# Kernel tuning notes

Hardware: AMD Instinct MI355X
Metric: run time of the kernel (lower is better)

Reference implementation:

```python
import jax, jax.numpy as jnp
import numpy as np

THETA = 10000.0
N_HEADS = 16


def setup_inputs() -> dict:
    key = jax.random.key(0)
    kx, kq, kk, kv, ko = jax.random.split(key, 5)
    B, S, D = 2, 2048, 1024
    std = np.sqrt(2.0 / (D + D))
    def mk_w(k):
        # trunc_normal in [-3*std, 3*std], stored as [in_features, out_features]
        return jax.random.truncated_normal(k, -3.0, 3.0, (D, D), jnp.float32) * std
    return {
        "x": jax.random.normal(kx, (B, S, D), dtype=jnp.float32),
        "token_positions": jnp.arange(S, dtype=jnp.int64) if jax.config.jax_enable_x64 else jnp.arange(S, dtype=jnp.int32),
        "WQ": mk_w(kq),
        "WK": mk_w(kk),
        "WV": mk_w(kv),
        "WO": mk_w(ko),
    }


def _rope(x, pos, theta):
    # x: [B, H, S, d_k]; pos: [S]
    d_k = x.shape[-1]
    freq = 1.0 / theta ** (jnp.arange(0, d_k, 2, dtype=jnp.float32) / d_k)  # [d_k//2]
    ang = pos.astype(jnp.float32)[:, None] * freq                            # [S, d_k//2]
    cos, sin = jnp.cos(ang), jnp.sin(ang)
    xp = x.reshape(x.shape[:-1] + (d_k // 2, 2))
    x0, x1 = xp[..., 0], xp[..., 1]
    r0 = cos * x0 - sin * x1
    r1 = sin * x0 + cos * x1
    return jnp.stack([r0, r1], axis=-1).reshape(x.shape)


def reference(x, token_positions, WQ, WK, WV, WO):
    B, S, D = x.shape
    H = N_HEADS
    dk = D // H
    # Linear in source computes y = x @ W.T (W stored [in, out], used transposed)
    def proj(W):
        return jnp.einsum('oi,bsi->bso', W, x).reshape(B, S, H, dk).transpose(0, 2, 1, 3)
    Q = proj(WQ)  # [B, H, S, dk]
    K = proj(WK)
    V = proj(WV)
    Q = _rope(Q, token_positions, THETA)
    K = _rope(K, token_positions, THETA)
    scores = jnp.einsum('bhqd,bhkd->bhqk', Q, K) / np.sqrt(dk).astype(np.float32)
    causal = jnp.tril(jnp.ones((S, S), dtype=bool))
    scores = jnp.where(causal, scores, jnp.float32(-1e9))
    w = jax.nn.softmax(scores, axis=-1)
    out = jnp.einsum('bhqk,bhkd->bhqd', w, V)
    out = out.transpose(0, 2, 1, 3).reshape(B, S, D)
    return jnp.einsum('oi,bsi->bso', WO, out)
```

## Files before the change

kernel.cpp:

```cpp
#include <hip/hip_runtime.h>
#include <hip/hip_bf16.h>

#define S_LEN   2048
#define D_MODEL 1024
#define NH      16
#define DKH     64
#define BATCH   2
#define BS_ROWS 4096

typedef unsigned short u16;
typedef __attribute__((ext_vector_type(4))) float f32x4;
typedef __attribute__((ext_vector_type(8))) short bf16x8;

__device__ __forceinline__ float bf2f(u16 u) {
  union { unsigned int i; float f; } v; v.i = ((unsigned int)u) << 16; return v.f;
}
__device__ __forceinline__ u16 f2bf(float f) {
  union { __hip_bfloat16 h; u16 u; } cv; cv.h = __float2bfloat16(f); return cv.u;
}
__device__ __forceinline__ f32x4 mfma16(bf16x8 a, bf16x8 b, f32x4 c) {
  return __builtin_amdgcn_mfma_f32_16x16x32_bf16(a, b, c, 0, 0, 0);
}
__device__ __forceinline__ void gl_lds16(const u16* g, u16* l) {
  __builtin_amdgcn_global_load_lds(
      (const __attribute__((address_space(1))) void*)g,
      (__attribute__((address_space(3))) void*)l, 16, 0, 0);
}

__global__ void cvt_all(const float* __restrict__ x,
                        const float* __restrict__ wq, const float* __restrict__ wk,
                        const float* __restrict__ wv, const float* __restrict__ wo,
                        u16* __restrict__ xb, u16* __restrict__ wqb, u16* __restrict__ wkb,
                        u16* __restrict__ wvb, u16* __restrict__ wob) {
  int seg = blockIdx.y;
  const float* src; u16* dst;
  if (seg < 4)      { src = x + (size_t)seg * (1u << 20); dst = xb + (size_t)seg * (1u << 20); }
  else if (seg == 4){ src = wq; dst = wqb; }
  else if (seg == 5){ src = wk; dst = wkb; }
  else if (seg == 6){ src = wv; dst = wvb; }
  else              { src = wo; dst = wob; }
  int i = blockIdx.x * 256 + threadIdx.x;
  float4 v = reinterpret_cast<const float4*>(src)[i];
  ushort4 o;
  o.x = f2bf(v.x); o.y = f2bf(v.y); o.z = f2bf(v.z); o.w = f2bf(v.w);
  reinterpret_cast<ushort4*>(dst)[i] = o;
}

#define BM 128
#define BN 128
#define BKK 64

__global__ __launch_bounds__(256) void gemm_bt(
    const u16* __restrict__ A,
    const u16* __restrict__ B0, const u16* __restrict__ B1, const u16* __restrict__ B2,
    u16* __restrict__ C0, u16* __restrict__ C1, u16* __restrict__ C2,
    float* __restrict__ Cf,
    int M, int N, int K, int out_f32)
{
  __shared__ __align__(16) u16 As[BM * BKK];
  __shared__ __align__(16) u16 Bs[BN * BKK];

  const int z = blockIdx.z;
  const u16* Bm = (z == 0) ? B0 : ((z == 1) ? B1 : B2);
  u16* Cb = (z == 0) ? C0 : ((z == 1) ? C1 : C2);

  const int tid = threadIdx.x;
  const int l = tid & 63, w = tid >> 6;
  const int lr = l & 15, lg = l >> 4;
  const int m0 = blockIdx.y * BM, n0 = blockIdx.x * BN;
  const int wr = w >> 1, wc = w & 1;

  f32x4 acc[4][4];
#pragma unroll
  for (int mi = 0; mi < 4; ++mi)
#pragma unroll
    for (int nj = 0; nj < 4; ++nj)
      acc[mi][nj] = (f32x4){0.f, 0.f, 0.f, 0.f};

  for (int k0 = 0; k0 < K; k0 += BKK) {
    __syncthreads();
#pragma unroll
    for (int i = 0; i < 4; ++i) {
      int Dc = w * 256 + i * 64 + l;
      int row = Dc >> 3;
      int c = (Dc & 7) ^ (row & 7);
      gl_lds16(A  + (size_t)(m0 + row) * K + k0 + c * 8, As + (w * 256 + i * 64) * 8);
      gl_lds16(Bm + (size_t)(n0 + row) * K + k0 + c * 8, Bs + (w * 256 + i * 64) * 8);
    }
    __syncthreads();

    bf16x8 af[2][4], bfr[2][4];
#pragma unroll
    for (int kk = 0; kk < 2; ++kk)
#pragma unroll
      for (int mi = 0; mi < 4; ++mi) {
        int rowa = wr * 64 + mi * 16 + lr;
        int ck = kk * 4 + lg;
        af[kk][mi] = *(const bf16x8*)&As[rowa * BKK + (((ck) ^ (rowa & 7)) << 3)];
        int rowb = wc * 64 + mi * 16 + lr;
        bfr[kk][mi] = *(const bf16x8*)&Bs[rowb * BKK + (((ck) ^ (rowb & 7)) << 3)];
      }
#pragma unroll
    for (int kk = 0; kk < 2; ++kk)
#pragma unroll
      for (int mi = 0; mi < 4; ++mi)
#pragma unroll
        for (int nj = 0; nj < 4; ++nj)
          acc[mi][nj] = mfma16(af[kk][mi], bfr[kk][nj], acc[mi][nj]);
  }

#pragma unroll
  for (int mi = 0; mi < 4; ++mi)
#pragma unroll
    for (int nj = 0; nj < 4; ++nj)
#pragma unroll
      for (int r = 0; r < 4; ++r) {
        int row = m0 + wr * 64 + mi * 16 + lg * 4 + r;
        int col = n0 + wc * 64 + nj * 16 + lr;
        float v = acc[mi][nj][r];
        if (out_f32) Cf[(size_t)row * N + col] = v;
        else         Cb[(size_t)row * N + col] = f2bf(v);
      }
}

__global__ void rope_pack(const u16* __restrict__ Yq, const u16* __restrict__ Yk,
                          const u16* __restrict__ Yv, const int* __restrict__ pos,
                          u16* __restrict__ Qb, u16* __restrict__ Kb, u16* __restrict__ Vt)
{
  int t = blockIdx.x * blockDim.x + threadIdx.x;
  if (t >= BS_ROWS * (D_MODEL / 2)) return;
  int pi = t & 511;
  int r  = t >> 9;
  int h = pi >> 5, j = pi & 31;
  int b = r >> 11, s = r & (S_LEN - 1);
  int p = pos[s];

  float freq = exp2f(-(float)j * 0.41524101186092028f);
  float ang = (float)p * freq;
  float sn, cs;
  sincosf(ang, &sn, &cs);

  int base = r * D_MODEL + pi * 2;
  float q0 = bf2f(Yq[base]), q1 = bf2f(Yq[base + 1]);
  float k0 = bf2f(Yk[base]), k1 = bf2f(Yk[base + 1]);
  float v0 = bf2f(Yv[base]), v1 = bf2f(Yv[base + 1]);

  const float QS = 0.18033688011112042f;
  float qr0 = (cs * q0 - sn * q1) * QS;
  float qr1 = (sn * q0 + cs * q1) * QS;
  float kr0 = cs * k0 - sn * k1;
  float kr1 = sn * k0 + cs * k1;

  int bh = b * NH + h;
  size_t qidx = ((size_t)bh * S_LEN + s) * DKH + 2 * j;
  ushort2 qo; qo.x = f2bf(qr0); qo.y = f2bf(qr1);
  ushort2 ko; ko.x = f2bf(kr0); ko.y = f2bf(kr1);
  *reinterpret_cast<ushort2*>(Qb + qidx) = qo;
  *reinterpret_cast<ushort2*>(Kb + qidx) = ko;
  Vt[((size_t)bh * DKH + 2 * j)     * S_LEN + s] = f2bf(v0);
  Vt[((size_t)bh * DKH + 2 * j + 1) * S_LEN + s] = f2bf(v1);
}

__global__ __launch_bounds__(256) void attn_fwd(
    const u16* __restrict__ Qb, const u16* __restrict__ Kb,
    const u16* __restrict__ Vt, u16* __restrict__ Ob)
{
  const int f = blockIdx.x;
  const int xcd = f & 7, slot = f >> 3;
  const int bh = xcd * 4 + (slot >> 4);
  const int p  = slot & 15;
  const int qbh = 31 - p, qbl = p;
  const int b = bh >> 4, h = bh & 15;
  const int tid = threadIdx.x, l = tid & 63, w = tid >> 6;
  const int lr = l & 15, lg = l >> 4;

  __shared__ __align__(16) u16 Ks[2][64 * 64];
  __shared__ __align__(16) u16 Vs[2][64 * 64];
  __shared__ __align__(16) u16 Ps[4][16 * 64];

  const u16* Qh = Qb + (size_t)bh * S_LEN * DKH;
  const u16* Kh = Kb + (size_t)bh * S_LEN * DKH;
  const u16* Vh = Vt + (size_t)bh * DKH * S_LEN;

  const int q0h = qbh * 64 + w * 16;
  const int q0l = qbl * 64 + w * 16;

  bf16x8 qfh[2], qfl[2];
#pragma unroll
  for (int kk = 0; kk < 2; ++kk) {
    qfh[kk] = *(const bf16x8*)(Qh + (size_t)(q0h + lr) * DKH + kk * 32 + lg * 8);
    qfl[kk] = *(const bf16x8*)(Qh + (size_t)(q0l + lr) * DKH + kk * 32 + lg * 8);
  }

  f32x4 oh[4], ol[4];
  float mh[4], ml[4], lh[4], ll[4];
#pragma unroll
  for (int r = 0; r < 4; ++r) {
    mh[r] = -INFINITY; ml[r] = -INFINITY; lh[r] = 0.f; ll[r] = 0.f;
  }
#pragma unroll
  for (int nb = 0; nb < 4; ++nb) {
    oh[nb] = (f32x4){0.f, 0.f, 0.f, 0.f};
    ol[nb] = (f32x4){0.f, 0.f, 0.f, 0.f};
  }

#define STAGE(buf, tt) do {                                                        \
    int kv0s = (tt) * 64;                                                          \
    _Pragma("unroll")                                                              \
    for (int i = 0; i < 2; ++i) {                                                  \
      int Dc = w * 128 + i * 64 + l;                                               \
      int row = Dc >> 3;                                                           \
      int c = (Dc & 7) ^ (row & 7);                                                \
      gl_lds16(Kh + (size_t)(kv0s + row) * DKH + c * 8, &Ks[buf][(w * 128 + i * 64) * 8]); \
      gl_lds16(Vh + (size_t)row * S_LEN + kv0s + c * 8, &Vs[buf][(w * 128 + i * 64) * 8]); \
    }                                                                              \
  } while (0)

  auto compute = [&](int cur, int kv0, const bf16x8 (&qf)[2], f32x4 (&oacc)[4],
                     float (&m)[4], float (&lsum)[4], int q0, bool diag) {
    f32x4 sf[4];
#pragma unroll
    for (int nj = 0; nj < 4; ++nj) {
      f32x4 a = (f32x4){0.f, 0.f, 0.f, 0.f};
#pragma unroll
      for (int kk = 0; kk < 2; ++kk) {
        int brow = nj * 16 + lr;
        bf16x8 kf = *(const bf16x8*)&Ks[cur][brow * 64 + (((kk * 4 + lg) ^ (brow & 7)) << 3)];
        a = mfma16(qf[kk], kf, a);
      }
      sf[nj] = a;
    }
    if (diag) {
#pragma unroll
      for (int nj = 0; nj < 4; ++nj)
#pragma unroll
        for (int r = 0; r < 4; ++r) {
          int colg = kv0 + nj * 16 + lr;
          int rowg = q0 + lg * 4 + r;
          if (colg > rowg) sf[nj][r] = -1e30f;
        }
    }
    float pm[4];
#pragma unroll
    for (int r = 0; r < 4; ++r) {
      float v = fmaxf(fmaxf(sf[0][r], sf[1][r]), fmaxf(sf[2][r], sf[3][r]));
      v = fmaxf(v, __shfl_xor(v, 1));
      v = fmaxf(v, __shfl_xor(v, 2));
      v = fmaxf(v, __shfl_xor(v, 4));
      v = fmaxf(v, __shfl_xor(v, 8));
      pm[r] = v;
    }
    bool need = false;
#pragma unroll
    for (int r = 0; r < 4; ++r) need = need || (pm[r] > m[r] + 8.f);
    if (__any(need)) {
#pragma unroll
      for (int r = 0; r < 4; ++r) {
        float mn = fmaxf(m[r], pm[r]);
        float sc = exp2f(m[r] - mn);
        m[r] = mn;
        lsum[r] *= sc;
#pragma unroll
        for (int nb = 0; nb < 4; ++nb) oacc[nb][r] *= sc;
      }
    }
    float ps[4] = {0.f, 0.f, 0.f, 0.f};
#pragma unroll
    for (int nj = 0; nj < 4; ++nj)
#pragma unroll
      for (int r = 0; r < 4; ++r) {
        float pv = exp2f(sf[nj][r] - m[r]);
        sf[nj][r] = pv;
        ps[r] += pv;
      }
#pragma unroll
    for (int r = 0; r < 4; ++r) lsum[r] += ps[r];

#pragma unroll
    for (int nj = 0; nj < 4; ++nj)
#pragma unroll
      for (int r = 0; r < 4; ++r) {
        int row = lg * 4 + r, col = nj * 16 + lr;
        int ck = col >> 3;
        Ps[w][row * 64 + ((ck ^ (row & 7)) << 3) + (col & 7)] = f2bf(sf[nj][r]);
      }
#pragma unroll
    for (int kk = 0; kk < 2; ++kk) {
      bf16x8 pa = *(const bf16x8*)&Ps[w][lr * 64 + (((kk * 4 + lg) ^ (lr & 7)) << 3)];
#pragma unroll
      for (int nb = 0; nb < 4; ++nb) {
        int vrow = nb * 16 + lr;
        bf16x8 vf = *(const bf16x8*)&Vs[cur][vrow * 64 + (((kk * 4 + lg) ^ (vrow & 7)) << 3)];
        oacc[nb] = mfma16(pa, vf, oacc[nb]);
      }
    }
  };

  const int nt = 32 - p;
  STAGE(0, 0);
  __syncthreads();
  int cur = 0;
  for (int t = 0; t < nt; ++t) {
    if (t + 1 < nt) STAGE(cur ^ 1, t + 1);
    const int kv0 = t * 64;
    compute(cur, kv0, qfh, oh, mh, lh, q0h, t == qbh);
    if (t <= p) compute(cur, kv0, qfl, ol, ml, ll, q0l, t == qbl);
    __syncthreads();
    cur ^= 1;
  }
#undef STAGE

  auto finish = [&](f32x4 (&oacc)[4], float (&lsum)[4], int q0) {
    float inv[4];
#pragma unroll
    for (int r = 0; r < 4; ++r) {
      float v = lsum[r];
      v += __shfl_xor(v, 1); v += __shfl_xor(v, 2);
      v += __shfl_xor(v, 4); v += __shfl_xor(v, 8);
      inv[r] = 1.0f / v;
    }
#pragma unroll
    for (int nb = 0; nb < 4; ++nb)
#pragma unroll
      for (int r = 0; r < 4; ++r) {
        int sg = q0 + lg * 4 + r;
        int dg = nb * 16 + lr;
        Ob[(size_t)b * S_LEN * D_MODEL + (size_t)sg * D_MODEL + h * DKH + dg] =
            f2bf(oacc[nb][r] * inv[r]);
      }
  };
  finish(oh, lh, q0h);
  finish(ol, ll, q0l);
}

extern "C" void kernel_launch(void* const* d_in, const int* in_sizes, int n_in,
                              void* d_out, int out_size, void* d_ws, size_t ws_size,
                              hipStream_t stream) {
  const float* x   = (const float*)d_in[0];
  const int*   pos = (const int*)d_in[1];
  const float* WQ  = (const float*)d_in[2];
  const float* WK  = (const float*)d_in[3];
  const float* WV  = (const float*)d_in[4];
  const float* WO  = (const float*)d_in[5];

  char* ws = (char*)d_ws;
  u16* xb  = (u16*)(ws);
  u16* wqb = (u16*)(ws + (size_t)(8)  * 1048576);
  u16* wkb = (u16*)(ws + (size_t)(10) * 1048576);
  u16* wvb = (u16*)(ws + (size_t)(12) * 1048576);
  u16* wob = (u16*)(ws + (size_t)(14) * 1048576);
  u16* Yq  = (u16*)(ws + (size_t)(16) * 1048576);
  u16* Yk  = (u16*)(ws + (size_t)(24) * 1048576);
  u16* Yv  = (u16*)(ws + (size_t)(32) * 1048576);
  u16* Qb  = (u16*)(ws + (size_t)(40) * 1048576);
  u16* Kb  = (u16*)(ws + (size_t)(48) * 1048576);
  u16* Vt  = (u16*)(ws + (size_t)(56) * 1048576);
  u16* Ob  = (u16*)(ws + (size_t)(64) * 1048576);

  cvt_all<<<dim3(1024, 8), 256, 0, stream>>>(x, WQ, WK, WV, WO, xb, wqb, wkb, wvb, wob);

  gemm_bt<<<dim3(D_MODEL / BN, BS_ROWS / BM, 3), 256, 0, stream>>>(
      xb, wqb, wkb, wvb, Yq, Yk, Yv, nullptr, BS_ROWS, D_MODEL, D_MODEL, 0);

  rope_pack<<<(BS_ROWS * (D_MODEL / 2)) / 256, 256, 0, stream>>>(
      Yq, Yk, Yv, pos, Qb, Kb, Vt);

  attn_fwd<<<dim3(512), 256, 0, stream>>>(Qb, Kb, Vt, Ob);

  gemm_bt<<<dim3(D_MODEL / BN, BS_ROWS / BM, 1), 256, 0, stream>>>(
      Ob, wob, wob, wob, nullptr, nullptr, nullptr, (float*)d_out,
      BS_ROWS, D_MODEL, D_MODEL, 1);
}
```

Before: 249.1 us.

## Split V transpose into tiled LDS kernel and use one query block per attention workgroup

The strided scatter of V into the transposed layout moves out of rope_pack into a dedicated LDS-tiled transpose kernel, so both its reads and its writes are coalesced. The attention kernel drops the paired high/low query-block scheme and instead launches 1024 workgroups, one 64-row query block each, ordered longest-first with a launch-bounds occupancy hint. This cuts per-block register pressure and raises parallelism, but each block loads its own K/V tiles, so pairs no longer share them. It also gives up the explicit XCD-aware head placement and adds one extra kernel launch.

After: 238.2 us. -4.4%, faster.

```diff
diff --git a/kernel.cpp b/kernel.cpp
--- a/kernel.cpp
+++ b/kernel.cpp
@@ -9,6 +9,7 @@
 #define BS_ROWS 4096
 
 typedef unsigned short u16;
+typedef unsigned int   u32;
 typedef __attribute__((ext_vector_type(4))) float f32x4;
 typedef __attribute__((ext_vector_type(8))) short bf16x8;
 
@@ -124,8 +125,8 @@
 }
 
 __global__ void rope_pack(const u16* __restrict__ Yq, const u16* __restrict__ Yk,
-                          const u16* __restrict__ Yv, const int* __restrict__ pos,
-                          u16* __restrict__ Qb, u16* __restrict__ Kb, u16* __restrict__ Vt)
+                          const int* __restrict__ pos,
+                          u16* __restrict__ Qb, u16* __restrict__ Kb)
 {
   int t = blockIdx.x * blockDim.x + threadIdx.x;
   if (t >= BS_ROWS * (D_MODEL / 2)) return;
@@ -143,7 +144,6 @@
   int base = r * D_MODEL + pi * 2;
   float q0 = bf2f(Yq[base]), q1 = bf2f(Yq[base + 1]);
   float k0 = bf2f(Yk[base]), k1 = bf2f(Yk[base + 1]);
-  float v0 = bf2f(Yv[base]), v1 = bf2f(Yv[base + 1]);
 
   const float QS = 0.18033688011112042f;
   float qr0 = (cs * q0 - sn * q1) * QS;
@@ -157,19 +157,46 @@
   ushort2 ko; ko.x = f2bf(kr0); ko.y = f2bf(kr1);
   *reinterpret_cast<ushort2*>(Qb + qidx) = qo;
   *reinterpret_cast<ushort2*>(Kb + qidx) = ko;
-  Vt[((size_t)bh * DKH + 2 * j)     * S_LEN + s] = f2bf(v0);
-  Vt[((size_t)bh * DKH + 2 * j + 1) * S_LEN + s] = f2bf(v1);
-}
-
-__global__ __launch_bounds__(256) void attn_fwd(
+}
+
+__global__ __launch_bounds__(256) void transpose_v(const u16* __restrict__ Yv,
+                                                   u16* __restrict__ Vt)
+{
+  __shared__ u32 T[64][65];
+  const int sb = blockIdx.x;
+  const int bh = blockIdx.y;
+  const int b = bh >> 4, h = bh & 15;
+  const int t = threadIdx.x;
+  const int s0 = sb * 64;
+
+#pragma unroll
+  for (int pass = 0; pass < 2; ++pass) {
+    int row = pass * 32 + (t >> 3);
+    int c0 = (t & 7) * 8;
+    bf16x8 v = *(const bf16x8*)(Yv + (size_t)(b * S_LEN + s0 + row) * D_MODEL + h * DKH + c0);
+#pragma unroll
+    for (int i = 0; i < 8; ++i) T[row][c0 + i] = (u32)(u16)v[i];
+  }
+  __syncthreads();
+
+  const int d = t >> 2, ch = t & 3;
+  bf16x8 o0, o1;
+#pragma unroll
+  for (int i = 0; i < 8; ++i) o0[i] = (short)(u16)T[ch * 16 + i][d];
+#pragma unroll
+  for (int i = 0; i < 8; ++i) o1[i] = (short)(u16)T[ch * 16 + 8 + i][d];
+  u16* dst = Vt + ((size_t)bh * DKH + d) * S_LEN + s0 + ch * 16;
+  *(bf16x8*)dst = o0;
+  *(bf16x8*)(dst + 8) = o1;
+}
+
+__global__ __launch_bounds__(256, 4) void attn_fwd(
     const u16* __restrict__ Qb, const u16* __restrict__ Kb,
     const u16* __restrict__ Vt, u16* __restrict__ Ob)
 {
   const int f = blockIdx.x;
-  const int xcd = f & 7, slot = f >> 3;
-  const int bh = xcd * 4 + (slot >> 4);
-  const int p  = slot & 15;
-  const int qbh = 31 - p, qbl = p;
+  const int qb = 31 - (f >> 5);
+  const int bh = f & 31;
   const int b = bh >> 4, h = bh & 15;
   const int tid = threadIdx.x, l = tid & 63, w = tid >> 6;
   const int lr = l & 15, lg = l >> 4;
@@ -182,27 +209,19 @@
   const u16* Kh = Kb + (size_t)bh * S_LEN * DKH;
   const u16* Vh = Vt + (size_t)bh * DKH * S_LEN;
 
-  const int q0h = qbh * 64 + w * 16;
-  const int q0l = qbl * 64 + w * 16;
-
-  bf16x8 qfh[2], qfl[2];
-#pragma unroll
-  for (int kk = 0; kk < 2; ++kk) {
-    qfh[kk] = *(const bf16x8*)(Qh + (size_t)(q0h + lr) * DKH + kk * 32 + lg * 8);
-    qfl[kk] = *(const bf16x8*)(Qh + (size_t)(q0l + lr) * DKH + kk * 32 + lg * 8);
-  }
-
-  f32x4 oh[4], ol[4];
-  float mh[4], ml[4], lh[4], ll[4];
-#pragma unroll
-  for (int r = 0; r < 4; ++r) {
-    mh[r] = -INFINITY; ml[r] = -INFINITY; lh[r] = 0.f; ll[r] = 0.f;
-  }
-#pragma unroll
-  for (int nb = 0; nb < 4; ++nb) {
-    oh[nb] = (f32x4){0.f, 0.f, 0.f, 0.f};
-    ol[nb] = (f32x4){0.f, 0.f, 0.f, 0.f};
-  }
+  const int q0 = qb * 64 + w * 16;
+
+  bf16x8 qf[2];
+#pragma unroll
+  for (int kk = 0; kk < 2; ++kk)
+    qf[kk] = *(const bf16x8*)(Qh + (size_t)(q0 + lr) * DKH + kk * 32 + lg * 8);
+
+  f32x4 oacc[4];
+  float m[4], lsum[4];
+#pragma unroll
+  for (int r = 0; r < 4; ++r) { m[r] = -INFINITY; lsum[r] = 0.f; }
+#pragma unroll
+  for (int nb = 0; nb < 4; ++nb) oacc[nb] = (f32x4){0.f, 0.f, 0.f, 0.f};
 
 #define STAGE(buf, tt) do {                                                        \
     int kv0s = (tt) * 64;                                                          \
@@ -216,8 +235,14 @@
     }                                                                              \
   } while (0)
 
-  auto compute = [&](int cur, int kv0, const bf16x8 (&qf)[2], f32x4 (&oacc)[4],
-                     float (&m)[4], float (&lsum)[4], int q0, bool diag) {
+  const int nt = qb + 1;
+  STAGE(0, 0);
+  __syncthreads();
+  int cur = 0;
+  for (int t = 0; t < nt; ++t) {
+    if (t + 1 < nt) STAGE(cur ^ 1, t + 1);
+    const int kv0 = t * 64;
+
     f32x4 sf[4];
 #pragma unroll
     for (int nj = 0; nj < 4; ++nj) {
@@ -230,7 +255,7 @@
       }
       sf[nj] = a;
     }
-    if (diag) {
+    if (t == qb) {
 #pragma unroll
       for (int nj = 0; nj < 4; ++nj)
 #pragma unroll
@@ -294,43 +319,29 @@
         oacc[nb] = mfma16(pa, vf, oacc[nb]);
       }
     }
-  };
-
-  const int nt = 32 - p;
-  STAGE(0, 0);
-  __syncthreads();
-  int cur = 0;
-  for (int t = 0; t < nt; ++t) {
-    if (t + 1 < nt) STAGE(cur ^ 1, t + 1);
-    const int kv0 = t * 64;
-    compute(cur, kv0, qfh, oh, mh, lh, q0h, t == qbh);
-    if (t <= p) compute(cur, kv0, qfl, ol, ml, ll, q0l, t == qbl);
+
     __syncthreads();
     cur ^= 1;
   }
 #undef STAGE
 
-  auto finish = [&](f32x4 (&oacc)[4], float (&lsum)[4], int q0) {
-    float inv[4];
+  float inv[4];
+#pragma unroll
+  for (int r = 0; r < 4; ++r) {
+    float v = lsum[r];
+    v += __shfl_xor(v, 1); v += __shfl_xor(v, 2);
+    v += __shfl_xor(v, 4); v += __shfl_xor(v, 8);
+    inv[r] = 1.0f / v;
+  }
+#pragma unroll
+  for (int nb = 0; nb < 4; ++nb)
 #pragma unroll
     for (int r = 0; r < 4; ++r) {
-      float v = lsum[r];
-      v += __shfl_xor(v, 1); v += __shfl_xor(v, 2);
-      v += __shfl_xor(v, 4); v += __shfl_xor(v, 8);
-      inv[r] = 1.0f / v;
-    }
-#pragma unroll
-    for (int nb = 0; nb < 4; ++nb)
-#pragma unroll
-      for (int r = 0; r < 4; ++r) {
-        int sg = q0 + lg * 4 + r;
-        int dg = nb * 16 + lr;
-        Ob[(size_t)b * S_LEN * D_MODEL + (size_t)sg * D_MODEL + h * DKH + dg] =
-            f2bf(oacc[nb][r] * inv[r]);
-      }
-  };
-  finish(oh, lh, q0h);
-  finish(ol, ll, q0l);
+      int sg = q0 + lg * 4 + r;
+      int dg = nb * 16 + lr;
+      Ob[(size_t)b * S_LEN * D_MODEL + (size_t)sg * D_MODEL + h * DKH + dg] =
+          f2bf(oacc[nb][r] * inv[r]);
+    }
 }
 
 extern "C" void kernel_launch(void* const* d_in, const int* in_sizes, int n_in,
@@ -363,9 +374,11 @@
       xb, wqb, wkb, wvb, Yq, Yk, Yv, nullptr, BS_ROWS, D_MODEL, D_MODEL, 0);
 
   rope_pack<<<(BS_ROWS * (D_MODEL / 2)) / 256, 256, 0, stream>>>(
-      Yq, Yk, Yv, pos, Qb, Kb, Vt);
-
-  attn_fwd<<<dim3(512), 256, 0, stream>>>(Qb, Kb, Vt, Ob);
+      Yq, Yk, pos, Qb, Kb);
+
+  transpose_v<<<dim3(S_LEN / 64, BATCH * NH), 256, 0, stream>>>(Yv, Vt);
+
+  attn_fwd<<<dim3(1024), 256, 0, stream>>>(Qb, Kb, Vt, Ob);
 
   gemm_bt<<<dim3(D_MODEL / BN, BS_ROWS / BM, 1), 256, 0, stream>>>(
       Ob, wob, wob, wob, nullptr, nullptr, nullptr, (float*)d_out,
```
